# Kernel optimization log

Hardware: AMD Instinct MI355X
Metric: run time of the kernel (lower is better)

Reference implementation:

```python
import jax, jax.numpy as jnp
import numpy as np


def setup_inputs() -> dict:
    key = jax.random.key(0)
    k1, k2, k3, k4, k5 = jax.random.split(key, 5)
    B, C, Q, E = 16, 2048, 128, 200
    x_contexts = jax.random.normal(k1, (B, C, E), dtype=jnp.float32)
    x_questions = jax.random.normal(k2, (B, Q, E), dtype=jnp.float32)
    # nn.Linear(3E, 1, bias=False) weight: (1, 3E)
    w_sim = jax.random.normal(k3, (1, 3 * E), dtype=jnp.float32) * (1.0 / np.sqrt(3 * E))
    # nn.Linear(4E, 128) weight: (128, 4E), bias: (128,)
    w_proj = jax.random.normal(k4, (128, 4 * E), dtype=jnp.float32) * (1.0 / np.sqrt(4 * E))
    b_proj = jax.random.normal(k5, (128,), dtype=jnp.float32) * 0.01
    return {"x_contexts": x_contexts, "x_questions": x_questions,
            "w_sim": w_sim, "w_proj": w_proj, "b_proj": b_proj}


def reference(x_contexts, x_questions, w_sim, w_proj, b_proj):
    E = x_contexts.shape[-1]
    # Decompose w_sim . [c; q; c*q] into three small contractions — same math,
    # avoids materializing the (B, C, Q, 3E) broadcast tensor of the original.
    w1, w2, w3 = w_sim[0, :E], w_sim[0, E:2 * E], w_sim[0, 2 * E:]
    s_c = jnp.einsum('bce,e->bc', x_contexts, w1)            # (B, C)
    s_q = jnp.einsum('bqe,e->bq', x_questions, w2)           # (B, Q)
    s_cq = jnp.einsum('bce,bqe->bcq', x_contexts * w3, x_questions)  # (B, C, Q)
    scores = s_cq + s_c[:, :, None] + s_q[:, None, :]        # (B, C, Q)

    S1 = jax.nn.softmax(scores, axis=-1)   # softmax over question words
    S2 = jax.nn.softmax(scores, axis=-2)   # softmax over context words

    c2q = jnp.einsum('bcq,bqe->bce', S1, x_questions)        # (B, C, E)
    # q2c = (S1 @ S2^T) @ contexts; contract small E last to keep (B,C,C) single pass
    S1S2T = jnp.einsum('bcq,bdq->bcd', S1, S2)               # (B, C, C)
    q2c = jnp.einsum('bcd,bde->bce', S1S2T, x_contexts)      # (B, C, E)

    feats = jnp.concatenate(
        [x_contexts, c2q, x_contexts * c2q, x_contexts * q2c], axis=-1)  # (B, C, 4E)
    return jnp.einsum('bcf,of->bco', feats, w_proj) + b_proj  # (B, C, 128)
```

## Files before the change

### kernel.cpp

```cpp
#include <hip/hip_runtime.h>
#include <hip/hip_bf16.h>

#define Bn 16
#define Cn 2048
#define Qn 128
#define En 200
#define Fn 800
#define On 128
#define EP 208
#define KP 224
#define XR 448
#define CP 232

typedef float f32x4 __attribute__((ext_vector_type(4)));
typedef __bf16 bf16x8 __attribute__((ext_vector_type(8)));

__device__ __forceinline__ unsigned short f2bf(float f) {
    union { float f; unsigned u; } v; v.f = f;
    unsigned r = v.u + 0x7FFF + ((v.u >> 16) & 1);
    return (unsigned short)(r >> 16);
}
__device__ __forceinline__ float bf2f(unsigned short h) {
    union { unsigned u; float f; } v; v.u = (unsigned)h << 16;
    return v.f;
}
__device__ __forceinline__ bf16x8 mul8(bf16x8 a, bf16x8 b) {
    bf16x8 o;
#pragma unroll
    for (int k = 0; k < 8; ++k) o[k] = (__bf16)((float)a[k] * (float)b[k]);
    return o;
}
__device__ __forceinline__ bf16x8 scale8(bf16x8 a, float s) {
    bf16x8 o;
#pragma unroll
    for (int k = 0; k < 8; ++k) o[k] = (__bf16)((float)a[k] * s);
    return o;
}

__global__ __launch_bounds__(256) void k_prep_all(const float* __restrict__ xq,
                                                  const float* __restrict__ wsim,
                                                  const float* __restrict__ wp,
                                                  const float* __restrict__ xc,
                                                  unsigned short* __restrict__ yqb,
                                                  float* __restrict__ s_q,
                                                  unsigned short* __restrict__ wpP,
                                                  unsigned short* __restrict__ xqaT,
                                                  unsigned short* __restrict__ xcb,
                                                  unsigned short* __restrict__ xcT) {
    int bx = blockIdx.x;
    if (bx < 512) {
        int wid = (bx * 256 + threadIdx.x) >> 6;
        int lane = threadIdx.x & 63;
        const float* xrow = xq + (size_t)wid * En;
        float s = 0.f;
        for (int e = lane; e < En; e += 64) {
            float x = xrow[e];
            yqb[(size_t)wid * En + e] = f2bf(x * wsim[400 + e] + wsim[e]);
            s += x * wsim[200 + e];
        }
        for (int i = 32; i; i >>= 1) s += __shfl_xor(s, i, 64);
        if (lane == 0) s_q[wid] = s;
    } else if (bx < 624) {
        int gid = (bx - 512) * 256 + threadIdx.x;
        int flat = gid * 4;
        int s = flat / (On * KP);
        int rem = flat % (On * KP);
        int o = rem / KP, k = rem % KP;
        ushort4 ov = {0, 0, 0, 0};
        if (k < 200) {
            float4 v = *(const float4*)(wp + (size_t)o * Fn + s * 200 + k);
            ov.x = f2bf(v.x); ov.y = f2bf(v.y); ov.z = f2bf(v.z); ov.w = f2bf(v.w);
        }
        *(ushort4*)(wpP + flat) = ov;
    } else if (bx < 752) {
        int lb = bx - 624;
        int et = lb & 3, qt = (lb >> 2) & 1, b = lb >> 3;
        int e0 = et * 64, q0 = qt * 64;
        int tid = threadIdx.x;
        __shared__ float t[64][65];
        for (int i = tid; i < 64 * 64; i += 256) {
            int qi = i >> 6, ei = i & 63;
            int e = e0 + ei;
            t[qi][ei] = (e < En) ? xq[((size_t)(b * Qn + q0 + qi)) * En + e] : 0.f;
        }
        __syncthreads();
        for (int i = tid; i < 64 * 64; i += 256) {
            int ei = i >> 6, qi = i & 63;
            int e = e0 + ei;
            if (e < En)
                xqaT[((size_t)(b * XR + e)) * Qn + q0 + qi] = f2bf(t[qi][ei]);
        }
        if (et == 3) {
            for (int i = tid; i < 24 * 64; i += 256) {
                int e = 200 + (i >> 6), q = q0 + (i & 63);
                xqaT[((size_t)(b * XR + e)) * Qn + q] = 0;
            }
            for (int i = tid; i < 24 * 64; i += 256) {
                int e = 424 + (i >> 6), q = q0 + (i & 63);
                xqaT[((size_t)(b * XR + e)) * Qn + q] = 0;
            }
        }
    } else {
        int lb = bx - 752;
        int ct = lb & 31, et = (lb >> 5) & 3, b = lb >> 7;
        int c0 = ct * 64, e0 = et * 64;
        int tid = threadIdx.x;
        __shared__ float t[64][65];
        for (int i = tid; i < 64 * 64; i += 256) {
            int ci = i >> 6, ei = i & 63;
            int e = e0 + ei;
            t[ci][ei] = (e < En) ? xc[((size_t)(b * Cn + c0 + ci)) * En + e] : 0.f;
        }
        __syncthreads();
        for (int i = tid; i < 64 * 16; i += 256) {
            int ci = i >> 4, g4 = (i & 15) * 4;
            int e = e0 + g4;
            if (e + 3 < En) {
                ushort4 o;
                o.x = f2bf(t[ci][g4]); o.y = f2bf(t[ci][g4 + 1]);
                o.z = f2bf(t[ci][g4 + 2]); o.w = f2bf(t[ci][g4 + 3]);
                *(ushort4*)(xcb + ((size_t)(b * Cn + c0 + ci)) * En + e) = o;
            }
        }
        for (int i = tid; i < 64 * 64; i += 256) {
            int ei = i >> 6, ci = i & 63;
            int e = e0 + ei;
            if (e < EP)
                xcT[((size_t)(b * EP + e)) * Cn + c0 + ci] = f2bf(t[ci][ei]);
        }
    }
}

__global__ __launch_bounds__(256) void k_scores_mfma(const unsigned short* __restrict__ xcb,
                                                     const unsigned short* __restrict__ yqb,
                                                     const float* __restrict__ s_q,
                                                     unsigned short* __restrict__ ET,
                                                     unsigned short* __restrict__ s1,
                                                     float* __restrict__ cpM,
                                                     float* __restrict__ cpS) {
    int b = blockIdx.y, blk = blockIdx.x, c0 = blk * 64;
    int w = threadIdx.x >> 6, lane = threadIdx.x & 63;
    int lrow = lane & 15, kg = lane >> 4;
    __shared__ float colm4[4][128];
    __shared__ float cols4[4][128];
    const unsigned short* Ab = xcb + ((size_t)(b * Cn + c0 + w * 16 + lrow)) * En + kg * 8;
    const unsigned short* Bb = yqb + ((size_t)(b * Qn + lrow)) * En + kg * 8;
    f32x4 acc[8] = {};
#pragma unroll
    for (int kc = 0; kc < 7; ++kc) {
        bool valid = (kc < 6) || (kg == 0);
        bf16x8 af = bf16x8{0,0,0,0,0,0,0,0};
        if (valid) af = *(const bf16x8*)(Ab + kc * 32);
        bf16x8 bfr[8];
#pragma unroll
        for (int j = 0; j < 8; ++j) {
            bfr[j] = bf16x8{0,0,0,0,0,0,0,0};
            if (valid) bfr[j] = *(const bf16x8*)(Bb + (size_t)j * 16 * En + kc * 32);
        }
#pragma unroll
        for (int j = 0; j < 8; ++j)
            acc[j] = __builtin_amdgcn_mfma_f32_16x16x32_bf16(af, bfr[j], acc[j], 0, 0, 0);
    }
#pragma unroll
    for (int j = 0; j < 8; ++j) {
        float sq = s_q[b * Qn + j * 16 + lrow];
#pragma unroll
        for (int r = 0; r < 4; ++r) acc[j][r] += sq;
    }
    float lm[8], ls[8];
#pragma unroll
    for (int j = 0; j < 8; ++j) {
        float m = fmaxf(fmaxf(acc[j][0], acc[j][1]), fmaxf(acc[j][2], acc[j][3]));
        m = fmaxf(m, __shfl_xor(m, 16, 64));
        m = fmaxf(m, __shfl_xor(m, 32, 64));
        lm[j] = m;
        float s = __expf(acc[j][0] - m) + __expf(acc[j][1] - m)
                + __expf(acc[j][2] - m) + __expf(acc[j][3] - m);
        s += __shfl_xor(s, 16, 64);
        s += __shfl_xor(s, 32, 64);
        ls[j] = s;
    }
    if (kg == 0) {
#pragma unroll
        for (int j = 0; j < 8; ++j) {
            colm4[w][j * 16 + lrow] = lm[j];
            cols4[w][j * 16 + lrow] = ls[j];
        }
    }
    __syncthreads();
    float mb[8];
#pragma unroll
    for (int j = 0; j < 8; ++j) {
        int q = j * 16 + lrow;
        float m = fmaxf(fmaxf(colm4[0][q], colm4[1][q]), fmaxf(colm4[2][q], colm4[3][q]));
        mb[j] = m;
        if (w == 0 && kg == 0) {
            float sb = cols4[0][q] * __expf(colm4[0][q] - m)
                     + cols4[1][q] * __expf(colm4[1][q] - m)
                     + cols4[2][q] * __expf(colm4[2][q] - m)
                     + cols4[3][q] * __expf(colm4[3][q] - m);
            cpM[(b * 32 + blk) * 128 + q] = m;
            cpS[(b * 32 + blk) * 128 + q] = sb;
        }
    }
#pragma unroll
    for (int j = 0; j < 8; ++j) {
        int q = j * 16 + lrow;
        ushort4 o;
        o.x = f2bf(__expf(acc[j][0] - mb[j]));
        o.y = f2bf(__expf(acc[j][1] - mb[j]));
        o.z = f2bf(__expf(acc[j][2] - mb[j]));
        o.w = f2bf(__expf(acc[j][3] - mb[j]));
        *(ushort4*)(ET + ((size_t)(b * Qn + q)) * Cn + c0 + w * 16 + kg * 4) = o;
    }
    size_t rowbase = (size_t)(b * Cn + c0 + w * 16 + kg * 4);
#pragma unroll
    for (int r = 0; r < 4; ++r) {
        float m = acc[0][r];
#pragma unroll
        for (int j = 1; j < 8; ++j) m = fmaxf(m, acc[j][r]);
        for (int d = 1; d < 16; d <<= 1) m = fmaxf(m, __shfl_xor(m, d, 64));
        float ssum = 0.f;
        float e[8];
#pragma unroll
        for (int j = 0; j < 8; ++j) {
            e[j] = __expf(acc[j][r] - m);
            ssum += e[j];
        }
        for (int d = 1; d < 16; d <<= 1) ssum += __shfl_xor(ssum, d, 64);
        float si = 1.f / ssum;
#pragma unroll
        for (int j = 0; j < 8; ++j)
            s1[(rowbase + r) * Qn + j * 16 + lrow] = f2bf(e[j] * si);
    }
}

__global__ __launch_bounds__(256) void k_a_part(const unsigned short* __restrict__ ET,
                                                const unsigned short* __restrict__ xcT,
                                                const float* __restrict__ cpM,
                                                const float* __restrict__ cpS,
                                                float* __restrict__ aP) {
    int mt = blockIdx.x, ks = blockIdx.y, b = blockIdx.z;
    int tid = threadIdx.x;
    int w = tid >> 6, lane = tid & 63;
    int lrow = lane & 15, kg = lane >> 4;
    __shared__ float colMs[128], colSis[128];
    if (tid < 128) {
        int q = tid;
        float m = -1e30f;
        for (int k = 0; k < 32; k++) m = fmaxf(m, cpM[(b * 32 + k) * 128 + q]);
        float s = 0.f;
        for (int k = 0; k < 32; k++) s += cpS[(b * 32 + k) * 128 + q] * __expf(cpM[(b * 32 + k) * 128 + q] - m);
        colMs[q] = m;
        colSis[q] = 1.f / s;
    }
    __syncthreads();
    int q0 = w * 16 + lrow, q1 = q0 + 64;
    int cb0 = ks * 8;
    float corr0[8], corr1[8];
#pragma unroll
    for (int i = 0; i < 8; ++i) {
        corr0[i] = __expf(cpM[(b * 32 + cb0 + i) * 128 + q0] - colMs[q0]) * colSis[q0];
        corr1[i] = __expf(cpM[(b * 32 + cb0 + i) * 128 + q1] - colMs[q1]) * colSis[q1];
    }
    const unsigned short* Ab = xcT + ((size_t)(b * EP + mt * 16 + lrow)) * Cn + ks * 512 + kg * 8;
    const unsigned short* B0 = ET + ((size_t)(b * Qn + q0)) * Cn + ks * 512 + kg * 8;
    const unsigned short* B1 = ET + ((size_t)(b * Qn + q1)) * Cn + ks * 512 + kg * 8;
    f32x4 acc0 = {}, acc1 = {};
#pragma unroll
    for (int kb = 0; kb < 4; ++kb) {
        bf16x8 af[4], bv0[4], bv1[4];
#pragma unroll
        for (int k4 = 0; k4 < 4; ++k4) {
            af[k4]  = *(const bf16x8*)(Ab + (kb * 4 + k4) * 32);
            bv0[k4] = *(const bf16x8*)(B0 + (kb * 4 + k4) * 32);
            bv1[k4] = *(const bf16x8*)(B1 + (kb * 4 + k4) * 32);
        }
#pragma unroll
        for (int k4 = 0; k4 < 4; ++k4) {
            bf16x8 s0 = scale8(bv0[k4], corr0[kb * 2 + (k4 >> 1)]);
            bf16x8 s1v = scale8(bv1[k4], corr1[kb * 2 + (k4 >> 1)]);
            acc0 = __builtin_amdgcn_mfma_f32_16x16x32_bf16(af[k4], s0, acc0, 0, 0, 0);
            acc1 = __builtin_amdgcn_mfma_f32_16x16x32_bf16(af[k4], s1v, acc1, 0, 0, 0);
        }
    }
    size_t ebase = (size_t)(b * 4 + ks) * EP + mt * 16 + kg * 4;
#pragma unroll
    for (int r = 0; r < 4; ++r) {
        aP[(ebase + r) * Qn + q0] = acc0[r];
        aP[(ebase + r) * Qn + q1] = acc1[r];
    }
}

__global__ void k_acomb2(const float* __restrict__ aP, unsigned short* __restrict__ xqaT) {
    int gid = blockIdx.x * 256 + threadIdx.x;
    if (gid >= Bn * En * Qn) return;
    int b = gid / (En * Qn), r = gid % (En * Qn);
    int e = r / Qn, q = r % Qn;
    float s = 0.f;
#pragma unroll
    for (int k = 0; k < 4; k++)
        s += aP[((size_t)(b * 4 + k) * EP + e) * Qn + q];
    xqaT[((size_t)(b * XR + 224 + e)) * Qn + q] = f2bf(s);
}

template<int NJ>
__device__ __forceinline__ void cq2(const unsigned short* __restrict__ s1t,
                                    const unsigned short* __restrict__ xrows,
                                    unsigned short* __restrict__ cbuf,
                                    int J0, int kg, int lrow) {
    f32x4 acc[NJ][4];
#pragma unroll
    for (int j = 0; j < NJ; ++j)
#pragma unroll
        for (int m = 0; m < 4; ++m) acc[j][m] = f32x4{0.f, 0.f, 0.f, 0.f};
#pragma unroll
    for (int kc = 0; kc < 4; ++kc) {
        bf16x8 a[4];
#pragma unroll
        for (int m = 0; m < 4; ++m)
            a[m] = *(const bf16x8*)(s1t + (m * 16 + lrow) * 136 + kg * 8 + kc * 32);
        bf16x8 bv[NJ];
#pragma unroll
        for (int j = 0; j < NJ; ++j)
            bv[j] = *(const bf16x8*)(xrows + ((size_t)((J0 + j) * 16 + lrow)) * Qn + kg * 8 + kc * 32);
#pragma unroll
        for (int j = 0; j < NJ; ++j)
#pragma unroll
            for (int m = 0; m < 4; ++m)
                acc[j][m] = __builtin_amdgcn_mfma_f32_16x16x32_bf16(a[m], bv[j], acc[j][m], 0, 0, 0);
    }
#pragma unroll
    for (int j = 0; j < NJ; ++j) {
        int col = (J0 + j) * 16 + lrow;
#pragma unroll
        for (int m = 0; m < 4; ++m)
#pragma unroll
            for (int r = 0; r < 4; ++r)
                cbuf[(m * 16 + kg * 4 + r) * CP + col] = f2bf(acc[j][m][r]);
    }
}

__global__ __launch_bounds__(512, 4) void k_tail(const unsigned short* __restrict__ s1,
                                                 const unsigned short* __restrict__ xqaT,
                                                 const unsigned short* __restrict__ xcb,
                                                 const unsigned short* __restrict__ wpP,
                                                 const float* __restrict__ bp,
                                                 float* __restrict__ out) {
    int b = blockIdx.y, c0 = blockIdx.x * 64;
    int tid = threadIdx.x;
    int w = tid >> 6, lane = tid & 63;
    int lrow = lane & 15, kg = lane >> 4;
    __shared__ unsigned short s1t[64 * 136];
    __shared__ unsigned short xbuf[64 * CP];
    __shared__ unsigned short cbuf[64 * CP];

    for (int i = tid; i < 64 * 16; i += 512) {
        int row = i >> 4, c8 = i & 15;
        *(bf16x8*)(s1t + row * 136 + c8 * 8) =
            *(const bf16x8*)(s1 + ((size_t)(b * Cn + c0 + row)) * Qn + c8 * 8);
    }
    for (int i = tid; i < 64 * 28; i += 512) {
        int row = i / 28, c8 = i % 28;
        bf16x8 v = bf16x8{0,0,0,0,0,0,0,0};
        if (c8 < 25) v = *(const bf16x8*)(xcb + ((size_t)(b * Cn + c0 + row)) * En + c8 * 8);
        *(bf16x8*)(xbuf + row * CP + c8 * 8) = v;
    }
    __syncthreads();

    f32x4 acc[4] = {};
    const unsigned short* xq_b = xqaT + (size_t)b * XR * Qn;

    if (w < 6)      cq2<2>(s1t, xq_b, cbuf, 2 * w, kg, lrow);
    else if (w == 6) cq2<1>(s1t, xq_b, cbuf, 12, kg, lrow);
    else             cq2<1>(s1t, xq_b, cbuf, 13, kg, lrow);

    {
        const unsigned short* B0 = wpP + ((size_t)(0 * On + w * 16 + lrow)) * KP + kg * 8;
        const unsigned short* A0 = xbuf + lrow * CP + kg * 8;
#pragma unroll
        for (int kc = 0; kc < 7; ++kc) {
            bf16x8 b0 = *(const bf16x8*)(B0 + kc * 32);
#pragma unroll
            for (int m = 0; m < 4; ++m) {
                bf16x8 af = *(const bf16x8*)(A0 + m * 16 * CP + kc * 32);
                acc[m] = __builtin_amdgcn_mfma_f32_16x16x32_bf16(af, b0, acc[m], 0, 0, 0);
            }
        }
    }
    __syncthreads();

    {
        const unsigned short* B1 = wpP + ((size_t)(1 * On + w * 16 + lrow)) * KP + kg * 8;
        const unsigned short* B2 = wpP + ((size_t)(2 * On + w * 16 + lrow)) * KP + kg * 8;
        const unsigned short* Ax = xbuf + lrow * CP + kg * 8;
        const unsigned short* Ac = cbuf + lrow * CP + kg * 8;
#pragma unroll
        for (int kc = 0; kc < 7; ++kc) {
            bf16x8 b1 = *(const bf16x8*)(B1 + kc * 32);
            bf16x8 b2 = *(const bf16x8*)(B2 + kc * 32);
#pragma unroll
            for (int m = 0; m < 4; ++m) {
                bf16x8 ac = *(const bf16x8*)(Ac + m * 16 * CP + kc * 32);
                bf16x8 ax = *(const bf16x8*)(Ax + m * 16 * CP + kc * 32);
                acc[m] = __builtin_amdgcn_mfma_f32_16x16x32_bf16(ac, b1, acc[m], 0, 0, 0);
                acc[m] = __builtin_amdgcn_mfma_f32_16x16x32_bf16(mul8(ax, ac), b2, acc[m], 0, 0, 0);
            }
        }
    }
    __syncthreads();

    if (w < 6)      cq2<2>(s1t, xq_b + (size_t)224 * Qn, cbuf, 2 * w, kg, lrow);
    else if (w == 6) cq2<1>(s1t, xq_b + (size_t)224 * Qn, cbuf, 12, kg, lrow);
    else             cq2<1>(s1t, xq_b + (size_t)224 * Qn, cbuf, 13, kg, lrow);
    __syncthreads();

    {
        const unsigned short* B3 = wpP + ((size_t)(3 * On + w * 16 + lrow)) * KP + kg * 8;
        const unsigned short* Ax = xbuf + lrow * CP + kg * 8;
        const unsigned short* Ac = cbuf + lrow * CP + kg * 8;
#pragma unroll
        for (int kc = 0; kc < 7; ++kc) {
            bf16x8 b3 = *(const bf16x8*)(B3 + kc * 32);
#pragma unroll
            for (int m = 0; m < 4; ++m) {
                bf16x8 ac = *(const bf16x8*)(Ac + m * 16 * CP + kc * 32);
                bf16x8 ax = *(const bf16x8*)(Ax + m * 16 * CP + kc * 32);
                acc[m] = __builtin_amdgcn_mfma_f32_16x16x32_bf16(mul8(ax, ac), b3, acc[m], 0, 0, 0);
            }
        }
    }

    int o = w * 16 + lrow;
    float bpv = bp[o];
#pragma unroll
    for (int m = 0; m < 4; ++m)
#pragma unroll
        for (int r = 0; r < 4; ++r)
            out[((size_t)(b * Cn + c0 + m * 16 + kg * 4 + r)) * On + o] = acc[m][r] + bpv;
}

extern "C" void kernel_launch(void* const* d_in, const int* in_sizes, int n_in,
                              void* d_out, int out_size, void* d_ws, size_t ws_size,
                              hipStream_t stream) {
    const float* xc = (const float*)d_in[0];
    const float* xq = (const float*)d_in[1];
    const float* wsim = (const float*)d_in[2];
    const float* wp = (const float*)d_in[3];
    const float* bp = (const float*)d_in[4];
    float* out = (float*)d_out;
    float* ws = (float*)d_ws;

    unsigned short* ET_bf   = (unsigned short*)ws;
    unsigned short* s1_bf   = (unsigned short*)(ws + 2097152);
    unsigned short* xc_bf   = (unsigned short*)(ws + 4194304);
    unsigned short* xcT_bf  = (unsigned short*)(ws + 7471104);
    unsigned short* yq_bf   = (unsigned short*)(ws + 10878976);
    unsigned short* xqaT_bf = (unsigned short*)(ws + 11083776);
    unsigned short* wpP_bf  = (unsigned short*)(ws + 11542528);
    float* s_q   = ws + 11599872;
    float* cpM   = ws + 11601920;
    float* cpS   = ws + 11667456;
    float* aP    = ws + 11732992;

    k_prep_all<<<2800, 256, 0, stream>>>(xq, wsim, wp, xc, yq_bf, s_q, wpP_bf, xqaT_bf, xc_bf, xcT_bf);
    k_scores_mfma<<<dim3(32, 16), 256, 0, stream>>>(xc_bf, yq_bf, s_q, ET_bf, s1_bf, cpM, cpS);
    k_a_part<<<dim3(13, 4, 16), 256, 0, stream>>>(ET_bf, xcT_bf, cpM, cpS, aP);
    k_acomb2<<<1600, 256, 0, stream>>>(aP, xqaT_bf);
    k_tail<<<dim3(32, 16), 512, 0, stream>>>(s1_bf, xqaT_bf, xc_bf, wpP_bf, bp, out);
}
```

Before: 98.86 us.

## Fuse split-K reduction into a_part and restructure tail projection buffers

The split-K partial kernel now assigns the four K slices to the four waves of one block and reduces them in shared memory, writing bf16 results directly. This removes the separate combine kernel and the fp32 partial buffer round trip. The tail kernel packs x and c2q into one shared buffer and precomputes the x*c2q and x*q2c products in place, so each projection segment is a plain MFMA loop over preloaded weights. The cost is more block-level synchronisation, an extra shared-memory pass and one fewer independent block per K slice in the fused kernel.

```diff
diff --git a/kernel.cpp b/kernel.cpp
--- a/kernel.cpp
+++ b/kernel.cpp
@@ -10,7 +10,7 @@
 #define EP 208
 #define KP 224
 #define XR 448
-#define CP 232
+#define BUFP 456
 
 typedef float f32x4 __attribute__((ext_vector_type(4)));
 typedef __bf16 bf16x8 __attribute__((ext_vector_type(8)));
@@ -235,16 +235,17 @@
     }
 }
 
-__global__ __launch_bounds__(256) void k_a_part(const unsigned short* __restrict__ ET,
-                                                const unsigned short* __restrict__ xcT,
-                                                const float* __restrict__ cpM,
-                                                const float* __restrict__ cpS,
-                                                float* __restrict__ aP) {
-    int mt = blockIdx.x, ks = blockIdx.y, b = blockIdx.z;
+__global__ __launch_bounds__(256) void k_a_fused(const unsigned short* __restrict__ ET,
+                                                 const unsigned short* __restrict__ xcT,
+                                                 const float* __restrict__ cpM,
+                                                 const float* __restrict__ cpS,
+                                                 unsigned short* __restrict__ xqaT) {
+    int mt = blockIdx.x, qp = blockIdx.y, b = blockIdx.z;
     int tid = threadIdx.x;
     int w = tid >> 6, lane = tid & 63;
     int lrow = lane & 15, kg = lane >> 4;
     __shared__ float colMs[128], colSis[128];
+    __shared__ float red[4][2][16][16];
     if (tid < 128) {
         int q = tid;
         float m = -1e30f;
@@ -255,17 +256,17 @@
         colSis[q] = 1.f / s;
     }
     __syncthreads();
-    int q0 = w * 16 + lrow, q1 = q0 + 64;
-    int cb0 = ks * 8;
+    int q0 = qp * 16 + lrow, q1 = q0 + 64;
     float corr0[8], corr1[8];
 #pragma unroll
     for (int i = 0; i < 8; ++i) {
-        corr0[i] = __expf(cpM[(b * 32 + cb0 + i) * 128 + q0] - colMs[q0]) * colSis[q0];
-        corr1[i] = __expf(cpM[(b * 32 + cb0 + i) * 128 + q1] - colMs[q1]) * colSis[q1];
-    }
-    const unsigned short* Ab = xcT + ((size_t)(b * EP + mt * 16 + lrow)) * Cn + ks * 512 + kg * 8;
-    const unsigned short* B0 = ET + ((size_t)(b * Qn + q0)) * Cn + ks * 512 + kg * 8;
-    const unsigned short* B1 = ET + ((size_t)(b * Qn + q1)) * Cn + ks * 512 + kg * 8;
+        int cb = w * 8 + i;
+        corr0[i] = __expf(cpM[(b * 32 + cb) * 128 + q0] - colMs[q0]) * colSis[q0];
+        corr1[i] = __expf(cpM[(b * 32 + cb) * 128 + q1] - colMs[q1]) * colSis[q1];
+    }
+    const unsigned short* Ab = xcT + ((size_t)(b * EP + mt * 16 + lrow)) * Cn + w * 512 + kg * 8;
+    const unsigned short* B0 = ET + ((size_t)(b * Qn + q0)) * Cn + w * 512 + kg * 8;
+    const unsigned short* B1 = ET + ((size_t)(b * Qn + q1)) * Cn + w * 512 + kg * 8;
     f32x4 acc0 = {}, acc1 = {};
 #pragma unroll
     for (int kb = 0; kb < 4; ++kb) {
@@ -284,32 +285,30 @@
             acc1 = __builtin_amdgcn_mfma_f32_16x16x32_bf16(af[k4], s1v, acc1, 0, 0, 0);
         }
     }
-    size_t ebase = (size_t)(b * 4 + ks) * EP + mt * 16 + kg * 4;
 #pragma unroll
     for (int r = 0; r < 4; ++r) {
-        aP[(ebase + r) * Qn + q0] = acc0[r];
-        aP[(ebase + r) * Qn + q1] = acc1[r];
-    }
-}
-
-__global__ void k_acomb2(const float* __restrict__ aP, unsigned short* __restrict__ xqaT) {
-    int gid = blockIdx.x * 256 + threadIdx.x;
-    if (gid >= Bn * En * Qn) return;
-    int b = gid / (En * Qn), r = gid % (En * Qn);
-    int e = r / Qn, q = r % Qn;
-    float s = 0.f;
-#pragma unroll
-    for (int k = 0; k < 4; k++)
-        s += aP[((size_t)(b * 4 + k) * EP + e) * Qn + q];
-    xqaT[((size_t)(b * XR + 224 + e)) * Qn + q] = f2bf(s);
+        red[w][0][kg * 4 + r][lrow] = acc0[r];
+        red[w][1][kg * 4 + r][lrow] = acc1[r];
+    }
+    __syncthreads();
+#pragma unroll
+    for (int t = 0; t < 2; ++t) {
+        int idx = tid + t * 256;
+        int half = idx >> 8, rem = idx & 255;
+        int row = rem >> 4, col = rem & 15;
+        float s = red[0][half][row][col] + red[1][half][row][col]
+                + red[2][half][row][col] + red[3][half][row][col];
+        int e = mt * 16 + row;
+        int q = qp * 16 + half * 64 + col;
+        if (e < En)
+            xqaT[((size_t)(b * XR + 224 + e)) * Qn + q] = f2bf(s);
+    }
 }
 
 template<int NJ>
-__device__ __forceinline__ void cq2(const unsigned short* __restrict__ s1t,
-                                    const unsigned short* __restrict__ xrows,
-                                    unsigned short* __restrict__ cbuf,
-                                    int J0, int kg, int lrow) {
-    f32x4 acc[NJ][4];
+__device__ __forceinline__ void cq2_regs(const unsigned short* __restrict__ s1t,
+                                         const unsigned short* __restrict__ xrows,
+                                         f32x4 (&acc)[NJ][4], int J0, int kg, int lrow) {
 #pragma unroll
     for (int j = 0; j < NJ; ++j)
 #pragma unroll
@@ -330,6 +329,15 @@
             for (int m = 0; m < 4; ++m)
                 acc[j][m] = __builtin_amdgcn_mfma_f32_16x16x32_bf16(a[m], bv[j], acc[j][m], 0, 0, 0);
     }
+}
+
+template<int NJ>
+__device__ __forceinline__ void cq2_store(const unsigned short* __restrict__ s1t,
+                                          const unsigned short* __restrict__ xrows,
+                                          unsigned short* __restrict__ dst,
+                                          int J0, int kg, int lrow) {
+    f32x4 acc[NJ][4];
+    cq2_regs<NJ>(s1t, xrows, acc, J0, kg, lrow);
 #pragma unroll
     for (int j = 0; j < NJ; ++j) {
         int col = (J0 + j) * 16 + lrow;
@@ -337,7 +345,41 @@
         for (int m = 0; m < 4; ++m)
 #pragma unroll
             for (int r = 0; r < 4; ++r)
-                cbuf[(m * 16 + kg * 4 + r) * CP + col] = f2bf(acc[j][m][r]);
+                dst[(m * 16 + kg * 4 + r) * BUFP + col] = f2bf(acc[j][m][r]);
+    }
+}
+
+template<int NJ>
+__device__ __forceinline__ void mul_scatter(unsigned short* __restrict__ buf,
+                                            f32x4 (&acc)[NJ][4], int J0, int kg, int lrow) {
+#pragma unroll
+    for (int j = 0; j < NJ; ++j) {
+        int col = (J0 + j) * 16 + lrow;
+#pragma unroll
+        for (int m = 0; m < 4; ++m)
+#pragma unroll
+            for (int r = 0; r < 4; ++r) {
+                int idx = (m * 16 + kg * 4 + r) * BUFP + col;
+                buf[idx] = f2bf(bf2f(buf[idx]) * acc[j][m][r]);
+            }
+    }
+}
+
+__device__ __forceinline__ void proj_seg(f32x4 (&acc)[4],
+                                         const unsigned short* __restrict__ Aseg,
+                                         const unsigned short* __restrict__ Bslot,
+                                         int kg, int lrow) {
+    bf16x8 bv[7];
+#pragma unroll
+    for (int kc = 0; kc < 7; ++kc)
+        bv[kc] = *(const bf16x8*)(Bslot + kg * 8 + kc * 32);
+#pragma unroll
+    for (int kc = 0; kc < 7; ++kc) {
+#pragma unroll
+        for (int m = 0; m < 4; ++m) {
+            bf16x8 af = *(const bf16x8*)(Aseg + (m * 16 + lrow) * BUFP + kg * 8 + kc * 32);
+            acc[m] = __builtin_amdgcn_mfma_f32_16x16x32_bf16(af, bv[kc], acc[m], 0, 0, 0);
+        }
     }
 }
 
@@ -352,8 +394,7 @@
     int w = tid >> 6, lane = tid & 63;
     int lrow = lane & 15, kg = lane >> 4;
     __shared__ unsigned short s1t[64 * 136];
-    __shared__ unsigned short xbuf[64 * CP];
-    __shared__ unsigned short cbuf[64 * CP];
+    __shared__ unsigned short buf[64 * BUFP];
 
     for (int i = tid; i < 64 * 16; i += 512) {
         int row = i >> 4, c8 = i & 15;
@@ -364,71 +405,52 @@
         int row = i / 28, c8 = i % 28;
         bf16x8 v = bf16x8{0,0,0,0,0,0,0,0};
         if (c8 < 25) v = *(const bf16x8*)(xcb + ((size_t)(b * Cn + c0 + row)) * En + c8 * 8);
-        *(bf16x8*)(xbuf + row * CP + c8 * 8) = v;
-    }
+        *(bf16x8*)(buf + row * BUFP + c8 * 8) = v;
+    }
+    __syncthreads();
+
+    const unsigned short* xq_b = xqaT + (size_t)b * XR * Qn;
+
+    if (w < 6)       cq2_store<2>(s1t, xq_b, buf + 224, 2 * w, kg, lrow);
+    else if (w == 6) cq2_store<1>(s1t, xq_b, buf + 224, 12, kg, lrow);
+    else             cq2_store<1>(s1t, xq_b, buf + 224, 13, kg, lrow);
     __syncthreads();
 
     f32x4 acc[4] = {};
-    const unsigned short* xq_b = xqaT + (size_t)b * XR * Qn;
-
-    if (w < 6)      cq2<2>(s1t, xq_b, cbuf, 2 * w, kg, lrow);
-    else if (w == 6) cq2<1>(s1t, xq_b, cbuf, 12, kg, lrow);
-    else             cq2<1>(s1t, xq_b, cbuf, 13, kg, lrow);
-
     {
-        const unsigned short* B0 = wpP + ((size_t)(0 * On + w * 16 + lrow)) * KP + kg * 8;
-        const unsigned short* A0 = xbuf + lrow * CP + kg * 8;
-#pragma unroll
-        for (int kc = 0; kc < 7; ++kc) {
-            bf16x8 b0 = *(const bf16x8*)(B0 + kc * 32);
-#pragma unroll
-            for (int m = 0; m < 4; ++m) {
-                bf16x8 af = *(const bf16x8*)(A0 + m * 16 * CP + kc * 32);
-                acc[m] = __builtin_amdgcn_mfma_f32_16x16x32_bf16(af, b0, acc[m], 0, 0, 0);
-            }
-        }
-    }
+        const unsigned short* Bo = wpP + ((size_t)(w * 16 + lrow)) * KP;
+        proj_seg(acc, buf,       Bo,                        kg, lrow);
+        proj_seg(acc, buf + 224, Bo + (size_t)1 * On * KP,  kg, lrow);
+    }
+
+    f32x4 aq2[2][4];
+    if (w < 6)       cq2_regs<2>(s1t, xq_b + (size_t)224 * Qn, aq2, 2 * w, kg, lrow);
+    else if (w == 6) { f32x4 t1[1][4]; cq2_regs<1>(s1t, xq_b + (size_t)224 * Qn, t1, 12, kg, lrow);
+                       aq2[0][0]=t1[0][0]; aq2[0][1]=t1[0][1]; aq2[0][2]=t1[0][2]; aq2[0][3]=t1[0][3]; }
+    else             { f32x4 t1[1][4]; cq2_regs<1>(s1t, xq_b + (size_t)224 * Qn, t1, 13, kg, lrow);
+                       aq2[0][0]=t1[0][0]; aq2[0][1]=t1[0][1]; aq2[0][2]=t1[0][2]; aq2[0][3]=t1[0][3]; }
+    __syncthreads();
+
+    for (int i = tid; i < 64 * 28; i += 512) {
+        int row = i / 28, c8 = i % 28;
+        unsigned short* fr = buf + row * BUFP;
+        bf16x8 x  = *(bf16x8*)(fr + c8 * 8);
+        bf16x8 c2 = *(bf16x8*)(fr + 224 + c8 * 8);
+        *(bf16x8*)(fr + 224 + c8 * 8) = mul8(x, c2);
+    }
+    __syncthreads();
+
+    if (w < 6)       mul_scatter<2>(buf, aq2, 2 * w, kg, lrow);
+    else if (w == 6) { f32x4 t1[1][4]; t1[0][0]=aq2[0][0]; t1[0][1]=aq2[0][1]; t1[0][2]=aq2[0][2]; t1[0][3]=aq2[0][3];
+                       mul_scatter<1>(buf, t1, 12, kg, lrow); }
+    else             { f32x4 t1[1][4]; t1[0][0]=aq2[0][0]; t1[0][1]=aq2[0][1]; t1[0][2]=aq2[0][2]; t1[0][3]=aq2[0][3];
+                       mul_scatter<1>(buf, t1, 13, kg, lrow); }
     __syncthreads();
 
     {
-        const unsigned short* B1 = wpP + ((size_t)(1 * On + w * 16 + lrow)) * KP + kg * 8;
-        const unsigned short* B2 = wpP + ((size_t)(2 * On + w * 16 + lrow)) * KP + kg * 8;
-        const unsigned short* Ax = xbuf + lrow * CP + kg * 8;
-        const unsigned short* Ac = cbuf + lrow * CP + kg * 8;
-#pragma unroll
-        for (int kc = 0; kc < 7; ++kc) {
-            bf16x8 b1 = *(const bf16x8*)(B1 + kc * 32);
-            bf16x8 b2 = *(const bf16x8*)(B2 + kc * 32);
-#pragma unroll
-            for (int m = 0; m < 4; ++m) {
-                bf16x8 ac = *(const bf16x8*)(Ac + m * 16 * CP + kc * 32);
-                bf16x8 ax = *(const bf16x8*)(Ax + m * 16 * CP + kc * 32);
-                acc[m] = __builtin_amdgcn_mfma_f32_16x16x32_bf16(ac, b1, acc[m], 0, 0, 0);
-                acc[m] = __builtin_amdgcn_mfma_f32_16x16x32_bf16(mul8(ax, ac), b2, acc[m], 0, 0, 0);
-            }
-        }
-    }
-    __syncthreads();
-
-    if (w < 6)      cq2<2>(s1t, xq_b + (size_t)224 * Qn, cbuf, 2 * w, kg, lrow);
-    else if (w == 6) cq2<1>(s1t, xq_b + (size_t)224 * Qn, cbuf, 12, kg, lrow);
-    else             cq2<1>(s1t, xq_b + (size_t)224 * Qn, cbuf, 13, kg, lrow);
-    __syncthreads();
-
-    {
-        const unsigned short* B3 = wpP + ((size_t)(3 * On + w * 16 + lrow)) * KP + kg * 8;
-        const unsigned short* Ax = xbuf + lrow * CP + kg * 8;
-        const unsigned short* Ac = cbuf + lrow * CP + kg * 8;
-#pragma unroll
-        for (int kc = 0; kc < 7; ++kc) {
-            bf16x8 b3 = *(const bf16x8*)(B3 + kc * 32);
-#pragma unroll
-            for (int m = 0; m < 4; ++m) {
-                bf16x8 ac = *(const bf16x8*)(Ac + m * 16 * CP + kc * 32);
-                bf16x8 ax = *(const bf16x8*)(Ax + m * 16 * CP + kc * 32);
-                acc[m] = __builtin_amdgcn_mfma_f32_16x16x32_bf16(mul8(ax, ac), b3, acc[m], 0, 0, 0);
-            }
-        }
+        const unsigned short* Bo = wpP + ((size_t)(w * 16 + lrow)) * KP;
+        proj_seg(acc, buf,       Bo + (size_t)3 * On * KP, kg, lrow);
+        proj_seg(acc, buf + 224, Bo + (size_t)2 * On * KP, kg, lrow);
     }
 
     int o = w * 16 + lrow;
@@ -461,11 +483,9 @@
     float* s_q   = ws + 11599872;
     float* cpM   = ws + 11601920;
     float* cpS   = ws + 11667456;
-    float* aP    = ws + 11732992;
 
     k_prep_all<<<2800, 256, 0, stream>>>(xq, wsim, wp, xc, yq_bf, s_q, wpP_bf, xqaT_bf, xc_bf, xcT_bf);
     k_scores_mfma<<<dim3(32, 16), 256, 0, stream>>>(xc_bf, yq_bf, s_q, ET_bf, s1_bf, cpM, cpS);
-    k_a_part<<<dim3(13, 4, 16), 256, 0, stream>>>(ET_bf, xcT_bf, cpM, cpS, aP);
-    k_acomb2<<<1600, 256, 0, stream>>>(aP, xqaT_bf);
+    k_a_fused<<<dim3(13, 4, 16), 256, 0, stream>>>(ET_bf, xcT_bf, cpM, cpS, xqaT_bf);
     k_tail<<<dim3(32, 16), 512, 0, stream>>>(s1_bf, xqaT_bf, xc_bf, wpP_bf, bp, out);
 }
```

New measurement: 93.04 us. 5.9% less time.
